# Kernel optimization log

Hardware: AMD Instinct MI355X
Metric: run time of the kernel (lower is better)

## Reference

```python
import jax, jax.numpy as jnp
import numpy as np

BIG = 1e10
RADIUS = 0.5
NSAMPLE = 1


def square_distance(src, dst):
    # src: [B,N,3], dst: [B,M,3] -> [B,N,M] squared euclidean distances
    d = -2.0 * jnp.einsum('bnc,bmc->bnm', src, dst)
    d = d + jnp.sum(src ** 2, -1)[:, :, None]
    d = d + jnp.sum(dst ** 2, -1)[:, None, :]
    return d


def farthest_point_sample(xyz, npoint):
    # xyz: [B,N,3]; returns int32 indices [B,npoint]
    B, N, _ = xyz.shape
    dist0 = jnp.full((B, N), BIG, dtype=xyz.dtype)
    far0 = jnp.argmax(xyz[:, :, 0], axis=1).astype(jnp.int32)

    def step(carry, _):
        dist, far = carry
        centroid = jnp.take_along_axis(xyz, far[:, None, None], axis=1)  # [B,1,3]
        d = jnp.sum((xyz - centroid) ** 2, -1)  # [B,N]
        dist = jnp.minimum(dist, d)
        new_far = jnp.argmax(dist, axis=-1).astype(jnp.int32)
        return (dist, new_far), far  # record PRE-update farthest, like the torch loop

    (_, _), centroids = jax.lax.scan(step, (dist0, far0), None, length=npoint)
    return centroids.T  # [B,npoint]


def index_points(points, idx):
    # points: [B,N,C], idx: [B,S] -> [B,S,C]
    return jnp.take_along_axis(points, idx[:, :, None], axis=1)


def query_ball_point(radius, nsample, xyz, new_xyz):
    # xyz: [B,N,3], new_xyz: [B,S,3] -> int32 [B,S,nsample]
    B, S, _ = new_xyz.shape
    N = xyz.shape[1]
    sqrdists = square_distance(new_xyz, xyz)  # [B,S,N]
    base = jnp.arange(N, dtype=jnp.int32)
    group_idx = jnp.where(sqrdists > radius ** 2, jnp.int32(N), base)  # [B,S,N]
    group_idx = jnp.sort(group_idx, axis=-1)[:, :, :nsample]
    group_first = jnp.broadcast_to(group_idx[:, :, :1], group_idx.shape)
    group_idx = jnp.where(group_idx == N, group_first, group_idx)
    return group_idx


def setup_inputs() -> dict:
    key = jax.random.key(0)
    k1, k2 = jax.random.split(key)
    B, N = 4, 16384
    xyz = jax.random.uniform(k1, (B, 3, N), dtype=jnp.float32)
    cls_label = jax.random.uniform(k2, (B, 16), dtype=jnp.float32)
    return {"xyz": xyz, "cls_label": cls_label, "npoint": 1024}


def reference(xyz, cls_label, npoint):
    pts = jnp.transpose(xyz, (0, 2, 1))  # [B,N,3]
    centroids = farthest_point_sample(pts, npoint)  # [B,S]
    new_xyz = index_points(pts, centroids)  # [B,S,3]
    idx = query_ball_point(RADIUS, NSAMPLE, pts, new_xyz)  # [B,S,1]
    return idx
```

## Files before the change

### kernel.cpp

```cpp
#include <hip/hip_runtime.h>


constexpr int   N_PTS  = 16384;
constexpr int   NPOINT = 1024;
constexpr int   BLOCK  = 1024;
constexpr int   KPT    = N_PTS / BLOCK;
constexpr int   NPAIR  = KPT / 2;
constexpr int   NWAVE  = BLOCK / 64;
constexpr float BIGF   = 1e10f;

typedef float v2f __attribute__((ext_vector_type(2)));

__device__ inline float wave_max_f32(float v) {
    int x = __float_as_int(v);
    int t;
    t = __builtin_amdgcn_update_dpp(x, x, 0x111, 0xf, 0xf, false);
    x = __float_as_int(fmaxf(__int_as_float(x), __int_as_float(t)));
    t = __builtin_amdgcn_update_dpp(x, x, 0x112, 0xf, 0xf, false);
    x = __float_as_int(fmaxf(__int_as_float(x), __int_as_float(t)));
    t = __builtin_amdgcn_update_dpp(x, x, 0x114, 0xf, 0xf, false);
    x = __float_as_int(fmaxf(__int_as_float(x), __int_as_float(t)));
    t = __builtin_amdgcn_update_dpp(x, x, 0x118, 0xf, 0xf, false);
    x = __float_as_int(fmaxf(__int_as_float(x), __int_as_float(t)));
    t = __builtin_amdgcn_update_dpp(x, x, 0x142, 0xa, 0xf, false);
    x = __float_as_int(fmaxf(__int_as_float(x), __int_as_float(t)));
    t = __builtin_amdgcn_update_dpp(x, x, 0x143, 0xc, 0xf, false);
    x = __float_as_int(fmaxf(__int_as_float(x), __int_as_float(t)));
    return __int_as_float(__builtin_amdgcn_readlane(x, 63));
}

__global__ __launch_bounds__(BLOCK) void fps_kernel(
    const float* __restrict__ xyz,
    int* __restrict__ cent)
{
#pragma clang fp contract(off)
    const int b    = blockIdx.x;
    const int tid  = threadIdx.x;
    const int wave = tid >> 6;
    const int lane = tid & 63;
    const int pb   = tid * KPT;

    const float* X = xyz + (size_t)b * 3 * N_PTS;
    const float* Y = X + N_PTS;
    const float* Z = X + 2 * N_PTS;

    v2f px[NPAIR], py[NPAIR], pz[NPAIR], dst[NPAIR];
#pragma unroll
    for (int j = 0; j < NPAIR; ++j) {
        px[j]  = *(const v2f*)(X + pb + 2 * j);
        py[j]  = *(const v2f*)(Y + pb + 2 * j);
        pz[j]  = *(const v2f*)(Z + pb + 2 * j);
        dst[j] = (v2f){BIGF, BIGF};
    }

    __shared__ uint2 s_red[2][NWAVE];

    auto block_argmax = [&](float val, int idx, int r) -> int {
        const float mv = wave_max_f32(val);
        const unsigned long long cand = __ballot(val == mv);
        const int fl   = __ffsll((long long)cand) - 1;
        const int widx = __builtin_amdgcn_readlane(idx, fl);
        const int buf  = r & 1;
        if (lane == 0) {
            s_red[buf][wave] = make_uint2(__float_as_uint(mv), (unsigned)widx);
        }
        __syncthreads();
        uint2 e0 = s_red[buf][0];
        float bv = __uint_as_float(e0.x);
        int   bi = (int)e0.y;
#pragma unroll
        for (int w = 1; w < NWAVE; ++w) {
            const uint2 e = s_red[buf][w];
            const float v = __uint_as_float(e.x);
            if (v > bv) { bv = v; bi = (int)e.y; }
        }
        return __builtin_amdgcn_readfirstlane(bi);
    };

    float bv = -1.0f;
    int   bi = 0;
#pragma unroll
    for (int j = 0; j < NPAIR; ++j) {
        if (px[j].x > bv) { bv = px[j].x; bi = pb + 2 * j; }
        if (px[j].y > bv) { bv = px[j].y; bi = pb + 2 * j + 1; }
    }
    int far = block_argmax(bv, bi, 0);

    for (int it = 0; it < NPOINT; ++it) {
        if (tid == 0) cent[b * NPOINT + it] = far;
        if (it == NPOINT - 1) break;

        const float cx = X[far];
        const float cy = Y[far];
        const float cz = Z[far];
        const v2f c2x = {cx, cx}, c2y = {cy, cy}, c2z = {cz, cz};

        float nbv = -1.0f;
        int   nbi = 0;
#pragma unroll
        for (int j = 0; j < NPAIR; ++j) {
            const v2f dx = px[j] - c2x;
            const v2f dy = py[j] - c2y;
            const v2f dz = pz[j] - c2z;
            const v2f d  = (dx * dx + dy * dy) + dz * dz;
            v2f nd;
            nd.x = fminf(dst[j].x, d.x);
            nd.y = fminf(dst[j].y, d.y);
            dst[j] = nd;
            if (nd.x > nbv) { nbv = nd.x; nbi = pb + 2 * j; }
            if (nd.y > nbv) { nbv = nd.y; nbi = pb + 2 * j + 1; }
        }
        far = block_argmax(nbv, nbi, it + 1);
    }
}

__global__ __launch_bounds__(256) void ballq_kernel(
    const float* __restrict__ xyz,
    const int* __restrict__ cent,
    int* __restrict__ out)
{
    const int gw   = (blockIdx.x * 256 + threadIdx.x) >> 6;
    const int lane = threadIdx.x & 63;
    const int b = gw / NPOINT;
    const int s = gw % NPOINT;

    const float* X = xyz + (size_t)b * 3 * N_PTS;
    const float* Y = X + N_PTS;
    const float* Z = X + 2 * N_PTS;

    const int ci = cent[b * NPOINT + s];
    const float cx = X[ci], cy = Y[ci], cz = Z[ci];
    const float cn = __fadd_rn(
        __fadd_rn(__fmul_rn(cx, cx), __fmul_rn(cy, cy)), __fmul_rn(cz, cz));

    int res = N_PTS;
    for (int base = 0; base < N_PTS; base += 64) {
        const int p = base + lane;
        const float x = X[p], y = Y[p], z = Z[p];
        const float dot = __fadd_rn(
            __fadd_rn(__fmul_rn(x, cx), __fmul_rn(y, cy)), __fmul_rn(z, cz));
        const float pn = __fadd_rn(
            __fadd_rn(__fmul_rn(x, x), __fmul_rn(y, y)), __fmul_rn(z, z));
        const float d = __fadd_rn(__fadd_rn(__fmul_rn(-2.0f, dot), cn), pn);
        const unsigned long long m = __ballot(!(d > 0.25f));
        if (m) {
            res = base + (__ffsll((long long)m) - 1);
            break;
        }
    }
    if (lane == 0) out[b * NPOINT + s] = res;
}

extern "C" void kernel_launch(void* const* d_in, const int* in_sizes, int n_in,
                              void* d_out, int out_size, void* d_ws, size_t ws_size,
                              hipStream_t stream) {
    const float* xyz = (const float*)d_in[0];
    const int B = in_sizes[1] / 16;
    int* out = (int*)d_out;

    int* cent = (ws_size >= (size_t)B * NPOINT * sizeof(int)) ? (int*)d_ws
                                                              : (int*)d_out;

    fps_kernel<<<B, BLOCK, 0, stream>>>(xyz, cent);
    ballq_kernel<<<B * NPOINT / 4, 256, 0, stream>>>(xyz, cent, out);
}
```

Before: 2.140 ms.

## Halve FPS block size and defer per-lane argmax index search to winning lane

Reduces the FPS block from 1024 to 512 threads, so each thread holds 32 points in registers and there are fewer waves in the cross-wave reduction. The per-point inner loop now tracks only a running max value instead of a compare-and-select on value and index. The index is recovered afterwards by a scan run only in the lane that holds the wave maximum. It adds a waves-per-eu hint and an empty asm barrier to keep the coordinates in registers. The risks are higher register pressure, a serial index scan on the critical path, and half as many threads doing the distance work.

```diff
diff --git a/kernel.cpp b/kernel.cpp
--- a/kernel.cpp
+++ b/kernel.cpp
@@ -3,7 +3,7 @@
 
 constexpr int   N_PTS  = 16384;
 constexpr int   NPOINT = 1024;
-constexpr int   BLOCK  = 1024;
+constexpr int   BLOCK  = 512;
 constexpr int   KPT    = N_PTS / BLOCK;
 constexpr int   NPAIR  = KPT / 2;
 constexpr int   NWAVE  = BLOCK / 64;
@@ -29,9 +29,10 @@
     return __int_as_float(__builtin_amdgcn_readlane(x, 63));
 }
 
-__global__ __launch_bounds__(BLOCK) void fps_kernel(
-    const float* __restrict__ xyz,
-    int* __restrict__ cent)
+__global__ __launch_bounds__(BLOCK)
+__attribute__((amdgpu_waves_per_eu(2, 2)))
+void fps_kernel(const float* __restrict__ xyz,
+                int* __restrict__ cent)
 {
 #pragma clang fp contract(off)
     const int b    = blockIdx.x;
@@ -55,15 +56,10 @@
 
     __shared__ uint2 s_red[2][NWAVE];
 
-    auto block_argmax = [&](float val, int idx, int r) -> int {
-        const float mv = wave_max_f32(val);
-        const unsigned long long cand = __ballot(val == mv);
-        const int fl   = __ffsll((long long)cand) - 1;
-        const int widx = __builtin_amdgcn_readlane(idx, fl);
-        const int buf  = r & 1;
-        if (lane == 0) {
+    auto cross_wave = [&](float mv, int widx, int r) -> int {
+        const int buf = r & 1;
+        if (lane == 0)
             s_red[buf][wave] = make_uint2(__float_as_uint(mv), (unsigned)widx);
-        }
         __syncthreads();
         uint2 e0 = s_red[buf][0];
         float bv = __uint_as_float(e0.x);
@@ -77,40 +73,65 @@
         return __builtin_amdgcn_readfirstlane(bi);
     };
 
-    float bv = -1.0f;
-    int   bi = 0;
+    int far;
+    {
+        float m = -1.0f;
 #pragma unroll
-    for (int j = 0; j < NPAIR; ++j) {
-        if (px[j].x > bv) { bv = px[j].x; bi = pb + 2 * j; }
-        if (px[j].y > bv) { bv = px[j].y; bi = pb + 2 * j + 1; }
+        for (int j = 0; j < NPAIR; ++j)
+            m = fmaxf(m, fmaxf(px[j].x, px[j].y));
+        const float mv = wave_max_f32(m);
+        const unsigned long long match = __ballot(m == mv);
+        const int fl = __ffsll((long long)match) - 1;
+        int idx = 0;
+        if (lane == fl) {
+#pragma unroll
+            for (int j = NPAIR - 1; j >= 0; --j) {
+                if (px[j].y == mv) idx = pb + 2 * j + 1;
+                if (px[j].x == mv) idx = pb + 2 * j;
+            }
+        }
+        idx = __builtin_amdgcn_readlane(idx, fl);
+        far = cross_wave(mv, idx, 0);
     }
-    int far = block_argmax(bv, bi, 0);
 
     for (int it = 0; it < NPOINT; ++it) {
         if (tid == 0) cent[b * NPOINT + it] = far;
         if (it == NPOINT - 1) break;
+
+#pragma unroll
+        for (int j = 0; j < NPAIR; ++j)
+            asm volatile("" : "+v"(px[j]), "+v"(py[j]), "+v"(pz[j]));
 
         const float cx = X[far];
         const float cy = Y[far];
         const float cz = Z[far];
         const v2f c2x = {cx, cx}, c2y = {cy, cy}, c2z = {cz, cz};
 
-        float nbv = -1.0f;
-        int   nbi = 0;
+        float m = -1.0f;
 #pragma unroll
         for (int j = 0; j < NPAIR; ++j) {
             const v2f dx = px[j] - c2x;
             const v2f dy = py[j] - c2y;
             const v2f dz = pz[j] - c2z;
             const v2f d  = (dx * dx + dy * dy) + dz * dz;
-            v2f nd;
-            nd.x = fminf(dst[j].x, d.x);
-            nd.y = fminf(dst[j].y, d.y);
-            dst[j] = nd;
-            if (nd.x > nbv) { nbv = nd.x; nbi = pb + 2 * j; }
-            if (nd.y > nbv) { nbv = nd.y; nbi = pb + 2 * j + 1; }
+            dst[j].x = fminf(dst[j].x, d.x);
+            dst[j].y = fminf(dst[j].y, d.y);
+            m = fmaxf(m, fmaxf(dst[j].x, dst[j].y));
         }
-        far = block_argmax(nbv, nbi, it + 1);
+
+        const float mv = wave_max_f32(m);
+        const unsigned long long match = __ballot(m == mv);
+        const int fl = __ffsll((long long)match) - 1;
+        int idx = 0;
+        if (lane == fl) {
+#pragma unroll
+            for (int j = NPAIR - 1; j >= 0; --j) {
+                if (dst[j].y == mv) idx = pb + 2 * j + 1;
+                if (dst[j].x == mv) idx = pb + 2 * j;
+            }
+        }
+        idx = __builtin_amdgcn_readlane(idx, fl);
+        far = cross_wave(mv, idx, it + 1);
     }
 }
 
```

New measurement: 1.955 ms. 1.09x faster.
